# Kernel tuning notes

Measured on AMD Instinct MI355X. Metric: run time of the kernel, lower is better.

The kernel has to match this reference:

```python
import jax, jax.numpy as jnp
import numpy as np
import math

D_MODEL = 1024
NUM_HEADS = 16
D_K = D_MODEL // NUM_HEADS
MAX_SEQ_LEN = 2048
THETA = 10000.0
BATCH = 2
SEQ = 2048


def setup_inputs() -> dict:
    key = jax.random.key(0)
    ks = jax.random.split(key, 5)
    std = math.sqrt(2.0 / (D_MODEL + D_MODEL))
    def w(k):
        return jnp.clip(std * jax.random.normal(k, (D_MODEL, D_MODEL), dtype=jnp.float32), -3 * std, 3 * std)
    return {
        "x": jax.random.normal(ks[0], (BATCH, SEQ, D_MODEL), dtype=jnp.float32),
        "token_positions": jnp.arange(SEQ, dtype=jnp.int32),
        "Wq": w(ks[1]),
        "Wk": w(ks[2]),
        "Wv": w(ks[3]),
        "Wo": w(ks[4]),
    }


def _rope_tables():
    inv_freq = 1.0 / THETA ** (jnp.arange(0, D_K, 2, dtype=jnp.float32) / D_K)  # [d_k/2]
    positions = jnp.arange(MAX_SEQ_LEN, dtype=jnp.float32)[:, None]             # [max_seq, 1]
    angles = positions * inv_freq                                               # [max_seq, d_k/2]
    return jnp.cos(angles), jnp.sin(angles)


def _apply_rope(x, cos, sin):
    # x: [..., seq, d_k]; cos/sin: [seq, d_k/2] (broadcast over leading dims)
    x1, x2 = x[..., ::2], x[..., 1::2]
    r1 = x1 * cos - x2 * sin
    r2 = x1 * sin + x2 * cos
    return jnp.stack((r1, r2), axis=-1).reshape(x.shape)


def reference(x, token_positions, Wq, Wk, Wv, Wo):
    B, S, D = x.shape
    def proj(W):
        y = jnp.einsum('bsd,od->bso', x, W)
        return y.reshape(B, S, NUM_HEADS, D_K).transpose(0, 2, 1, 3)  # [B,H,S,dk]
    q, k, v = proj(Wq), proj(Wk), proj(Wv)

    cos_t, sin_t = _rope_tables()
    cos, sin = cos_t[token_positions], sin_t[token_positions]  # [S, d_k/2]
    q = _apply_rope(q, cos, sin)
    k = _apply_rope(k, cos, sin)

    scores = jnp.einsum('bhqd,bhkd->bhqk', q, k) / math.sqrt(D_K)
    causal = jnp.tril(jnp.ones((S, S), dtype=bool))
    scores = jnp.where(causal, scores, -jnp.inf)
    attn = jax.nn.softmax(scores, axis=-1)
    out = jnp.einsum('bhqk,bhkd->bhqd', attn, v)
    out = out.transpose(0, 2, 1, 3).reshape(B, S, D)
    return jnp.einsum('bsd,od->bso', out, Wo)
```

## Files before the change

### kernel.cpp

```cpp
#include <hip/hip_runtime.h>
#include <hip/hip_bf16.h>


typedef __attribute__((ext_vector_type(8))) short short8;
typedef __attribute__((ext_vector_type(4))) float floatx4;

static __device__ __forceinline__ unsigned short f2bf(float f) {
  __hip_bfloat16 h = __float2bfloat16(f);
  return *(unsigned short*)&h;
}

static __device__ __forceinline__ unsigned int pk2bf(float a, float b) {
  unsigned int ua = __float_as_uint(a) + 0x8000u;
  unsigned int ub = __float_as_uint(b) + 0x8000u;
  return __builtin_amdgcn_perm(ub, ua, 0x07060302u);
}

static __device__ __forceinline__ float fexp2(float x) {
  float r;
  asm("v_exp_f32 %0, %1\n\ts_nop 0" : "=v"(r) : "v"(x));
  return r;
}

static __device__ __forceinline__ void gl2lds16(const unsigned short* g,
                                                unsigned short* l) {
  __builtin_amdgcn_global_load_lds(
      (const __attribute__((address_space(1))) void*)g,
      (__attribute__((address_space(3))) void*)l, 16, 0, 0);
}

__global__ __launch_bounds__(256) void cvt_all(
    const float4* __restrict__ x,  const float4* __restrict__ wq,
    const float4* __restrict__ wk, const float4* __restrict__ wv,
    const float4* __restrict__ wo,
    ushort4* __restrict__ xb,  ushort4* __restrict__ wqb,
    ushort4* __restrict__ wkb, ushort4* __restrict__ wvb,
    ushort4* __restrict__ wob,
    const int* __restrict__ tokpos,
    float* __restrict__ ctab, float* __restrict__ stab) {
  int t = blockIdx.y;
  int i = blockIdx.x * 256 + threadIdx.x;
  if (t == 5) {
    if (i < 65536) {
      int s = i >> 5, f = i & 31;
      float inv = expf(-9.210340371976184f * (float)(2 * f) / 64.0f);
      float ang = (float)tokpos[s] * inv;
      ctab[i] = cosf(ang);
      stab[i] = sinf(ang);
    }
    return;
  }
  const float4* s = (t == 0) ? x : (t == 1) ? wq : (t == 2) ? wk : (t == 3) ? wv : wo;
  ushort4* d = (t == 0) ? xb : (t == 1) ? wqb : (t == 2) ? wkb : (t == 3) ? wvb : wob;
  int n4 = (t == 0) ? 1048576 : 262144;
  if (i < n4) {
    float4 v = s[i];
    ushort4 o;
    o.x = f2bf(v.x); o.y = f2bf(v.y); o.z = f2bf(v.z); o.w = f2bf(v.w);
    d[i] = o;
  }
}

#define GEMM128_BODY(Aptr, Wptr, m0, n0)                                        \
  __shared__ __align__(16) unsigned short lA[128 * 64];                         \
  __shared__ __align__(16) unsigned short lB[128 * 64];                         \
  int tid = threadIdx.x;                                                        \
  int wave = tid >> 6, lane = tid & 63;                                         \
  int wm = wave >> 1, wn = wave & 1;                                            \
  int l15 = lane & 15, quad = lane >> 4;                                        \
  int srow = wave * 32 + (lane >> 3);                   \
  int sch = lane & 7;                                   \
  int fsw = l15 & 7;                                 \
  floatx4 acc[4][4];                                                            \
  _Pragma("unroll") for (int m = 0; m < 4; ++m)                                 \
      _Pragma("unroll") for (int n = 0; n < 4; ++n)                             \
          acc[m][n] = (floatx4){0.f, 0.f, 0.f, 0.f};                            \
  for (int kt = 0; kt < 16; ++kt) {                                             \
    _Pragma("unroll") for (int p = 0; p < 4; ++p) {                             \
      int r = srow + p * 8;                                                     \
      int g = sch ^ (r & 7);                                                    \
      gl2lds16(Aptr + (size_t)(m0 + r) * 1024 + kt * 64 + g * 8,                \
               lA + (wave * 32 + p * 8) * 64);                                  \
      gl2lds16(Wptr + (size_t)(n0 + r) * 1024 + kt * 64 + g * 8,                \
               lB + (wave * 32 + p * 8) * 64);                                  \
    }                                                                           \
    __syncthreads();                                                            \
    _Pragma("unroll") for (int ks = 0; ks < 2; ++ks) {                          \
      short8 af[4], bf[4];                                                      \
      _Pragma("unroll") for (int m = 0; m < 4; ++m)                             \
          af[m] = *(const short8*)(lA + (wm * 64 + m * 16 + l15) * 64 +         \
                                   (((ks * 4 + quad) ^ fsw) * 8));              \
      _Pragma("unroll") for (int n = 0; n < 4; ++n)                             \
          bf[n] = *(const short8*)(lB + (wn * 64 + n * 16 + l15) * 64 +         \
                                   (((ks * 4 + quad) ^ fsw) * 8));              \
      _Pragma("unroll") for (int m = 0; m < 4; ++m)                             \
          _Pragma("unroll") for (int n = 0; n < 4; ++n)                         \
              acc[m][n] = __builtin_amdgcn_mfma_f32_16x16x32_bf16(              \
                  af[m], bf[n], acc[m][n], 0, 0, 0);                            \
    }                                                                           \
    __syncthreads();                                                            \
  }

__global__ __launch_bounds__(256) void qkv_mfma(
    const unsigned short* __restrict__ X,
    const unsigned short* __restrict__ Wq,
    const unsigned short* __restrict__ Wk,
    const unsigned short* __restrict__ Wv,
    const float* __restrict__ ctab, const float* __restrict__ stab,
    unsigned short* __restrict__ Qo, unsigned short* __restrict__ Ko,
    unsigned short* __restrict__ Vo) {
  int mat = blockIdx.z;
  const unsigned short* W = (mat == 0) ? Wq : ((mat == 1) ? Wk : Wv);
  unsigned short* Out = (mat == 0) ? Qo : ((mat == 1) ? Ko : Vo);
  int m0 = blockIdx.x * 128, n0 = blockIdx.y * 128;

  GEMM128_BODY(X, W, m0, n0)

#pragma unroll
  for (int n = 0; n < 4; ++n) {
    int col = n0 + wn * 64 + n * 16 + l15;
    int h = col >> 6;
    int d = col & 63;
    int pi = d >> 1;
    bool odd = (d & 1) != 0;
    size_t hb = (size_t)h * 2048 * 64;
#pragma unroll
    for (int m = 0; m < 4; ++m) {
      int row0 = m0 + wm * 64 + m * 16 + quad * 4;
      int b = row0 >> 11;
      int s0 = row0 & 2047;
      size_t base = (size_t)b * 16 * 2048 * 64 + hb;
      if (mat == 2) {
        ushort4 pv;
        pv.x = f2bf(acc[m][n][0]);
        pv.y = f2bf(acc[m][n][1]);
        pv.z = f2bf(acc[m][n][2]);
        pv.w = f2bf(acc[m][n][3]);
        *(ushort4*)(Out + base + (size_t)d * 2048 + s0) = pv;
      } else {
#pragma unroll
        for (int i = 0; i < 4; ++i) {
          int s = s0 + i;
          float v = acc[m][n][i];
          float p = __shfl_xor(v, 1);
          float c = ctab[s * 32 + pi];
          float sn = stab[s * 32 + pi];
          float res = odd ? fmaf(p, sn, v * c) : fmaf(v, c, -p * sn);
          if (mat == 0) res *= 0.1803368801111204f;
          Out[base + (size_t)s * 64 + d] = f2bf(res);
        }
      }
    }
  }
}

__global__ __launch_bounds__(256) void oproj_mfma(
    const unsigned short* __restrict__ A, const unsigned short* __restrict__ Wo,
    float* __restrict__ Out) {
  __shared__ __align__(16) unsigned short lA[64 * 64];
  __shared__ __align__(16) unsigned short lB[128 * 64];
  int tid = threadIdx.x;
  int wave = tid >> 6, lane = tid & 63;
  int l15 = lane & 15, quad = lane >> 4;
  int rsub = lane >> 3, sch = lane & 7;
  int fsw = l15 & 7;
  int m0 = blockIdx.x * 64, n0 = blockIdx.y * 128;

  floatx4 acc[4][2];
#pragma unroll
  for (int m = 0; m < 4; ++m)
#pragma unroll
    for (int n = 0; n < 2; ++n) acc[m][n] = (floatx4){0.f, 0.f, 0.f, 0.f};

  for (int kt = 0; kt < 16; ++kt) {
#pragma unroll
    for (int p = 0; p < 2; ++p) {
      int r = wave * 16 + p * 8 + rsub;
      int g = sch ^ (r & 7);
      gl2lds16(A + (size_t)(m0 + r) * 1024 + kt * 64 + g * 8,
               lA + (wave * 16 + p * 8) * 64);
    }
#pragma unroll
    for (int p = 0; p < 4; ++p) {
      int r = wave * 32 + p * 8 + rsub;
      int g = sch ^ (r & 7);
      gl2lds16(Wo + (size_t)(n0 + r) * 1024 + kt * 64 + g * 8,
               lB + (wave * 32 + p * 8) * 64);
    }
    __syncthreads();
#pragma unroll
    for (int ks = 0; ks < 2; ++ks) {
      int slot = ((ks * 4 + quad) ^ fsw) * 8;
      short8 af[4], bf[2];
#pragma unroll
      for (int m = 0; m < 4; ++m)
        af[m] = *(const short8*)(lA + (m * 16 + l15) * 64 + slot);
#pragma unroll
      for (int n = 0; n < 2; ++n)
        bf[n] = *(const short8*)(lB + (wave * 32 + n * 16 + l15) * 64 + slot);
#pragma unroll
      for (int m = 0; m < 4; ++m)
#pragma unroll
        for (int n = 0; n < 2; ++n)
          acc[m][n] = __builtin_amdgcn_mfma_f32_16x16x32_bf16(
              af[m], bf[n], acc[m][n], 0, 0, 0);
    }
    __syncthreads();
  }

#pragma unroll
  for (int m = 0; m < 4; ++m) {
#pragma unroll
    for (int n = 0; n < 2; ++n) {
      int col = n0 + wave * 32 + n * 16 + l15;
#pragma unroll
      for (int i = 0; i < 4; ++i) {
        int row = m0 + m * 16 + quad * 4 + i;
        Out[(size_t)row * 1024 + col] = acc[m][n][i];
      }
    }
  }
}

#define LPS 72

__global__ __launch_bounds__(256) void attn_flash(
    const unsigned short* __restrict__ Q, const unsigned short* __restrict__ K,
    const unsigned short* __restrict__ Vt, unsigned short* __restrict__ Oc) {
  __shared__ __align__(16) unsigned short lK[64 * 64];
  __shared__ __align__(16) unsigned short lV[64 * 64];
  __shared__ unsigned short lP[4][16 * LPS];

  int tid = threadIdx.x;
  int wave = tid >> 6, lane = tid & 63;
  int l15 = lane & 15, quad = lane >> 4;

  int xb_ = blockIdx.x;
  int yb_ = blockIdx.y;
  int jb = yb_ >> 3, ib = yb_ & 7;
  int qtile;
  if (jb == 0)      qtile = xb_;
  else if (jb == 1) qtile = 31 - xb_;
  else if (jb == 2) qtile = (15 - xb_) & 31;
  else              qtile = (16 + xb_) & 31;
  int bh = ib * 4 + jb;

  size_t base = (size_t)bh * 2048 * 64;
  int qbase = qtile * 64;

  const unsigned short* qrow = Q + base + (size_t)(qbase + wave * 16 + l15) * 64;
  short8 qb0 = *(const short8*)(qrow + quad * 8);
  short8 qb1 = *(const short8*)(qrow + 32 + quad * 8);

  floatx4 o[4];
  float m_i = -1e30f, l_i = 0.f;
#pragma unroll
  for (int n = 0; n < 4; ++n) o[n] = (floatx4){0.f, 0.f, 0.f, 0.f};

  int r0 = tid >> 3, g = tid & 7;
  int r1 = r0 + 32;
  int e0 = g * 8;
  int sl = (g ^ (r0 & 7)) * 8;
  int fsw = l15 & 7;
  int c0 = (quad ^ fsw) * 8;
  int c1 = ((quad + 4) ^ fsw) * 8;

  const unsigned short* kp = K + base;
  const unsigned short* vp = Vt + base;
  short8 pk0 = *(const short8*)(kp + r0 * 64 + e0);
  short8 pk1 = *(const short8*)(kp + r1 * 64 + e0);
  short8 pv0 = *(const short8*)(vp + (size_t)r0 * 2048 + e0);
  short8 pv1 = *(const short8*)(vp + (size_t)r1 * 2048 + e0);

  for (int kt = 0; kt <= qtile; ++kt) {
    __syncthreads();
    *(short8*)(lK + r0 * 64 + sl) = pk0;
    *(short8*)(lK + r1 * 64 + sl) = pk1;
    *(short8*)(lV + r0 * 64 + sl) = pv0;
    *(short8*)(lV + r1 * 64 + sl) = pv1;
    __syncthreads();

    if (kt < qtile) {
      const unsigned short* kn = K + base + (size_t)(kt + 1) * 4096;
      const unsigned short* vn = Vt + base + (kt + 1) * 64;
      pk0 = *(const short8*)(kn + r0 * 64 + e0);
      pk1 = *(const short8*)(kn + r1 * 64 + e0);
      pv0 = *(const short8*)(vn + (size_t)r0 * 2048 + e0);
      pv1 = *(const short8*)(vn + (size_t)r1 * 2048 + e0);
    }

    float sc[4][4];
#pragma unroll
    for (int sub = 0; sub < 4; ++sub) {
      const unsigned short* kr = lK + (sub * 16 + l15) * 64;
      short8 a0 = *(const short8*)(kr + c0);
      short8 a1 = *(const short8*)(kr + c1);
      floatx4 s = {0.f, 0.f, 0.f, 0.f};
      s = __builtin_amdgcn_mfma_f32_16x16x32_bf16(a0, qb0, s, 0, 0, 0);
      s = __builtin_amdgcn_mfma_f32_16x16x32_bf16(a1, qb1, s, 0, 0, 0);
#pragma unroll
      for (int i = 0; i < 4; ++i) sc[sub][i] = s[i];
    }

    if (kt == qtile) {
      int qin = wave * 16 + l15;
#pragma unroll
      for (int sub = 0; sub < 4; ++sub)
#pragma unroll
        for (int i = 0; i < 4; ++i)
          if (sub * 16 + quad * 4 + i > qin) sc[sub][i] = -1e30f;
    }

    float mb = sc[0][0];
#pragma unroll
    for (int sub = 0; sub < 4; ++sub)
#pragma unroll
      for (int i = 0; i < 4; ++i) mb = fmaxf(mb, sc[sub][i]);
    mb = fmaxf(mb, __shfl_xor(mb, 16));
    mb = fmaxf(mb, __shfl_xor(mb, 32));

    float mn = fmaxf(m_i, mb);
    float al = fexp2(m_i - mn);
    m_i = mn;
    float rs = 0.f;
#pragma unroll
    for (int sub = 0; sub < 4; ++sub)
#pragma unroll
      for (int i = 0; i < 4; ++i) {
        float p = fexp2(sc[sub][i] - mn);
        sc[sub][i] = p;
        rs += p;
      }
    rs += __shfl_xor(rs, 16);
    rs += __shfl_xor(rs, 32);
    l_i = l_i * al + rs;

#pragma unroll
    for (int n = 0; n < 4; ++n) {
      o[n][0] *= al; o[n][1] *= al; o[n][2] *= al; o[n][3] *= al;
    }

    unsigned short* pw = lP[wave] + l15 * LPS;
#pragma unroll
    for (int sub = 0; sub < 4; ++sub) {
      uint2 w;
      w.x = pk2bf(sc[sub][0], sc[sub][1]);
      w.y = pk2bf(sc[sub][2], sc[sub][3]);
      *(uint2*)(pw + sub * 16 + quad * 4) = w;
    }

    const unsigned short* pr = lP[wave] + l15 * LPS + quad * 8;
    short8 pa0 = *(const short8*)(pr);
    short8 pa1 = *(const short8*)(pr + 32);

#pragma unroll
    for (int n = 0; n < 4; ++n) {
      const unsigned short* vr = lV + (n * 16 + l15) * 64;
      short8 vb0 = *(const short8*)(vr + c0);
      short8 vb1 = *(const short8*)(vr + c1);
      o[n] = __builtin_amdgcn_mfma_f32_16x16x32_bf16(vb0, pa0, o[n], 0, 0, 0);
      o[n] = __builtin_amdgcn_mfma_f32_16x16x32_bf16(vb1, pa1, o[n], 0, 0, 0);
    }
  }

  int b = bh >> 4, h = bh & 15;
  float inv = 1.f / l_i;
  int s = qbase + wave * 16 + l15;
  size_t orow = (size_t)(b * 2048 + s) * 1024 + h * 64;
#pragma unroll
  for (int n = 0; n < 4; ++n) {
    uint2 ov;
    ov.x = pk2bf(o[n][0] * inv, o[n][1] * inv);
    ov.y = pk2bf(o[n][2] * inv, o[n][3] * inv);
    *(uint2*)(Oc + orow + n * 16 + quad * 4) = ov;
  }
}

extern "C" void kernel_launch(void* const* d_in, const int* in_sizes, int n_in,
                              void* d_out, int out_size, void* d_ws, size_t ws_size,
                              hipStream_t stream) {
  const float* x  = (const float*)d_in[0];
  const int* tokpos = (const int*)d_in[1];
  const float* Wq = (const float*)d_in[2];
  const float* Wk = (const float*)d_in[3];
  const float* Wv = (const float*)d_in[4];
  const float* Wo = (const float*)d_in[5];
  float* out = (float*)d_out;

  float* ws = (float*)d_ws;
  float* ctab = ws;
  float* stab = ctab + 65536;
  unsigned short* u = (unsigned short*)(stab + 65536);
  unsigned short* Qb  = u;
  unsigned short* Kb  = Qb + 4194304;
  unsigned short* Vb  = Kb + 4194304;
  unsigned short* Oc  = Vb + 4194304;
  unsigned short* xb  = Oc + 4194304;
  unsigned short* Wqb = xb + 4194304;
  unsigned short* Wkb = Wqb + 1048576;
  unsigned short* Wvb = Wkb + 1048576;
  unsigned short* Wob = Wvb + 1048576;

  cvt_all<<<dim3(4096, 6), 256, 0, stream>>>(
      (const float4*)x, (const float4*)Wq, (const float4*)Wk,
      (const float4*)Wv, (const float4*)Wo,
      (ushort4*)xb, (ushort4*)Wqb, (ushort4*)Wkb, (ushort4*)Wvb, (ushort4*)Wob,
      tokpos, ctab, stab);

  qkv_mfma<<<dim3(32, 8, 3), 256, 0, stream>>>(
      xb, Wqb, Wkb, Wvb, ctab, stab, Qb, Kb, Vb);
  attn_flash<<<dim3(32, 32), 256, 0, stream>>>(Qb, Kb, Vb, Oc);
  oproj_mfma<<<dim3(64, 8), 256, 0, stream>>>(Oc, Wob, out);
}
```

Baseline: 190.4 us.

## Load K and V fragments directly from global memory, dropping LDS staging

The attention kernel no longer stages K and V tiles through shared memory with block-wide barriers and register prefetch. Each wave now loads its MFMA operand fragments for K and V^T straight from global memory every iteration. This removes two __syncthreads per tile and the LDS traffic, but each of the four waves now fetches the same K/V data separately, relying on cache for reuse. It also loses the software prefetch of the next tile, so global latency is exposed inside the loop.

```diff
diff --git a/kernel.cpp b/kernel.cpp
--- a/kernel.cpp
+++ b/kernel.cpp
@@ -227,8 +227,6 @@
 __global__ __launch_bounds__(256) void attn_flash(
     const unsigned short* __restrict__ Q, const unsigned short* __restrict__ K,
     const unsigned short* __restrict__ Vt, unsigned short* __restrict__ Oc) {
-  __shared__ __align__(16) unsigned short lK[64 * 64];
-  __shared__ __align__(16) unsigned short lV[64 * 64];
   __shared__ unsigned short lP[4][16 * LPS];
 
   int tid = threadIdx.x;
@@ -257,47 +255,33 @@
 #pragma unroll
   for (int n = 0; n < 4; ++n) o[n] = (floatx4){0.f, 0.f, 0.f, 0.f};
 
-  int r0 = tid >> 3, g = tid & 7;
-  int r1 = r0 + 32;
-  int e0 = g * 8;
-  int sl = (g ^ (r0 & 7)) * 8;
-  int fsw = l15 & 7;
-  int c0 = (quad ^ fsw) * 8;
-  int c1 = ((quad + 4) ^ fsw) * 8;
-
-  const unsigned short* kp = K + base;
-  const unsigned short* vp = Vt + base;
-  short8 pk0 = *(const short8*)(kp + r0 * 64 + e0);
-  short8 pk1 = *(const short8*)(kp + r1 * 64 + e0);
-  short8 pv0 = *(const short8*)(vp + (size_t)r0 * 2048 + e0);
-  short8 pv1 = *(const short8*)(vp + (size_t)r1 * 2048 + e0);
+  const unsigned short* kfrag = K + base + (size_t)(l15)*64 + quad * 8;
+  const unsigned short* vfrag = Vt + base + (size_t)(l15)*2048 + quad * 8;
 
   for (int kt = 0; kt <= qtile; ++kt) {
-    __syncthreads();
-    *(short8*)(lK + r0 * 64 + sl) = pk0;
-    *(short8*)(lK + r1 * 64 + sl) = pk1;
-    *(short8*)(lV + r0 * 64 + sl) = pv0;
-    *(short8*)(lV + r1 * 64 + sl) = pv1;
-    __syncthreads();
-
-    if (kt < qtile) {
-      const unsigned short* kn = K + base + (size_t)(kt + 1) * 4096;
-      const unsigned short* vn = Vt + base + (kt + 1) * 64;
-      pk0 = *(const short8*)(kn + r0 * 64 + e0);
-      pk1 = *(const short8*)(kn + r1 * 64 + e0);
-      pv0 = *(const short8*)(vn + (size_t)r0 * 2048 + e0);
-      pv1 = *(const short8*)(vn + (size_t)r1 * 2048 + e0);
+    int k0 = kt * 64;
+
+    short8 ka0[4], ka1[4];
+#pragma unroll
+    for (int sub = 0; sub < 4; ++sub) {
+      const unsigned short* kr = kfrag + (size_t)(k0 + sub * 16) * 64;
+      ka0[sub] = *(const short8*)(kr);
+      ka1[sub] = *(const short8*)(kr + 32);
+    }
+    short8 va0[4], va1[4];
+#pragma unroll
+    for (int n = 0; n < 4; ++n) {
+      const unsigned short* vr = vfrag + (size_t)(n * 16) * 2048 + k0;
+      va0[n] = *(const short8*)(vr);
+      va1[n] = *(const short8*)(vr + 32);
     }
 
     float sc[4][4];
 #pragma unroll
     for (int sub = 0; sub < 4; ++sub) {
-      const unsigned short* kr = lK + (sub * 16 + l15) * 64;
-      short8 a0 = *(const short8*)(kr + c0);
-      short8 a1 = *(const short8*)(kr + c1);
       floatx4 s = {0.f, 0.f, 0.f, 0.f};
-      s = __builtin_amdgcn_mfma_f32_16x16x32_bf16(a0, qb0, s, 0, 0, 0);
-      s = __builtin_amdgcn_mfma_f32_16x16x32_bf16(a1, qb1, s, 0, 0, 0);
+      s = __builtin_amdgcn_mfma_f32_16x16x32_bf16(ka0[sub], qb0, s, 0, 0, 0);
+      s = __builtin_amdgcn_mfma_f32_16x16x32_bf16(ka1[sub], qb1, s, 0, 0, 0);
 #pragma unroll
       for (int i = 0; i < 4; ++i) sc[sub][i] = s[i];
     }
@@ -355,11 +339,8 @@
 
 #pragma unroll
     for (int n = 0; n < 4; ++n) {
-      const unsigned short* vr = lV + (n * 16 + l15) * 64;
-      short8 vb0 = *(const short8*)(vr + c0);
-      short8 vb1 = *(const short8*)(vr + c1);
-      o[n] = __builtin_amdgcn_mfma_f32_16x16x32_bf16(vb0, pa0, o[n], 0, 0, 0);
-      o[n] = __builtin_amdgcn_mfma_f32_16x16x32_bf16(vb1, pa1, o[n], 0, 0, 0);
+      o[n] = __builtin_amdgcn_mfma_f32_16x16x32_bf16(va0[n], pa0, o[n], 0, 0, 0);
+      o[n] = __builtin_amdgcn_mfma_f32_16x16x32_bf16(va1[n], pa1, o[n], 0, 0, 0);
     }
   }
 
```

Result: slower. 265.2 us (+39.3%).

## Double-buffer K/V tiles in LDS and swizzle P scratch layout

Applied to the files above, without the earlier changes.

The attention loop now keeps two LDS buffers for K and V. The next tile is written into the alternate buffer after the current tile's compute, so each iteration needs one barrier instead of two. The per-wave P scratch also drops its padded stride in favour of an XOR-swizzled 64-wide layout, to cut LDS bank conflicts on the P write and read. The cost is double the K/V LDS footprint, which may lower occupancy.

```diff
diff --git a/kernel.cpp b/kernel.cpp
--- a/kernel.cpp
+++ b/kernel.cpp
@@ -222,14 +222,12 @@
   }
 }
 
-#define LPS 72
-
 __global__ __launch_bounds__(256) void attn_flash(
     const unsigned short* __restrict__ Q, const unsigned short* __restrict__ K,
     const unsigned short* __restrict__ Vt, unsigned short* __restrict__ Oc) {
-  __shared__ __align__(16) unsigned short lK[64 * 64];
-  __shared__ __align__(16) unsigned short lV[64 * 64];
-  __shared__ unsigned short lP[4][16 * LPS];
+  __shared__ __align__(16) unsigned short lK[2][64 * 64];
+  __shared__ __align__(16) unsigned short lV[2][64 * 64];
+  __shared__ __align__(16) unsigned short lP[4][16 * 64];
 
   int tid = threadIdx.x;
   int wave = tid >> 6, lane = tid & 63;
@@ -265,22 +263,27 @@
   int c0 = (quad ^ fsw) * 8;
   int c1 = ((quad + 4) ^ fsw) * 8;
 
-  const unsigned short* kp = K + base;
-  const unsigned short* vp = Vt + base;
-  short8 pk0 = *(const short8*)(kp + r0 * 64 + e0);
-  short8 pk1 = *(const short8*)(kp + r1 * 64 + e0);
-  short8 pv0 = *(const short8*)(vp + (size_t)r0 * 2048 + e0);
-  short8 pv1 = *(const short8*)(vp + (size_t)r1 * 2048 + e0);
+  short8 pk0, pk1, pv0, pv1;
+  {
+    const unsigned short* kp = K + base;
+    const unsigned short* vp = Vt + base;
+    pk0 = *(const short8*)(kp + r0 * 64 + e0);
+    pk1 = *(const short8*)(kp + r1 * 64 + e0);
+    pv0 = *(const short8*)(vp + (size_t)r0 * 2048 + e0);
+    pv1 = *(const short8*)(vp + (size_t)r1 * 2048 + e0);
+    *(short8*)(lK[0] + r0 * 64 + sl) = pk0;
+    *(short8*)(lK[0] + r1 * 64 + sl) = pk1;
+    *(short8*)(lV[0] + r0 * 64 + sl) = pv0;
+    *(short8*)(lV[0] + r1 * 64 + sl) = pv1;
+  }
+  __syncthreads();
 
   for (int kt = 0; kt <= qtile; ++kt) {
-    __syncthreads();
-    *(short8*)(lK + r0 * 64 + sl) = pk0;
-    *(short8*)(lK + r1 * 64 + sl) = pk1;
-    *(short8*)(lV + r0 * 64 + sl) = pv0;
-    *(short8*)(lV + r1 * 64 + sl) = pv1;
-    __syncthreads();
-
-    if (kt < qtile) {
+    const unsigned short* kcur = lK[kt & 1];
+    const unsigned short* vcur = lV[kt & 1];
+    bool more = (kt < qtile);
+
+    if (more) {
       const unsigned short* kn = K + base + (size_t)(kt + 1) * 4096;
       const unsigned short* vn = Vt + base + (kt + 1) * 64;
       pk0 = *(const short8*)(kn + r0 * 64 + e0);
@@ -292,7 +295,7 @@
     float sc[4][4];
 #pragma unroll
     for (int sub = 0; sub < 4; ++sub) {
-      const unsigned short* kr = lK + (sub * 16 + l15) * 64;
+      const unsigned short* kr = kcur + (sub * 16 + l15) * 64;
       short8 a0 = *(const short8*)(kr + c0);
       short8 a1 = *(const short8*)(kr + c1);
       floatx4 s = {0.f, 0.f, 0.f, 0.f};
@@ -340,26 +343,37 @@
       o[n][0] *= al; o[n][1] *= al; o[n][2] *= al; o[n][3] *= al;
     }
 
-    unsigned short* pw = lP[wave] + l15 * LPS;
+    unsigned short* pw = lP[wave] + l15 * 64;
 #pragma unroll
     for (int sub = 0; sub < 4; ++sub) {
+      int pc = (((sub << 1) | (quad >> 1)) ^ fsw) * 8 + (quad & 1) * 4;
       uint2 w;
       w.x = pk2bf(sc[sub][0], sc[sub][1]);
       w.y = pk2bf(sc[sub][2], sc[sub][3]);
-      *(uint2*)(pw + sub * 16 + quad * 4) = w;
-    }
-
-    const unsigned short* pr = lP[wave] + l15 * LPS + quad * 8;
-    short8 pa0 = *(const short8*)(pr);
-    short8 pa1 = *(const short8*)(pr + 32);
+      *(uint2*)(pw + pc) = w;
+    }
+
+    const unsigned short* pr = lP[wave] + l15 * 64;
+    short8 pa0 = *(const short8*)(pr + c0);
+    short8 pa1 = *(const short8*)(pr + c1);
 
 #pragma unroll
     for (int n = 0; n < 4; ++n) {
-      const unsigned short* vr = lV + (n * 16 + l15) * 64;
+      const unsigned short* vr = vcur + (n * 16 + l15) * 64;
       short8 vb0 = *(const short8*)(vr + c0);
       short8 vb1 = *(const short8*)(vr + c1);
       o[n] = __builtin_amdgcn_mfma_f32_16x16x32_bf16(vb0, pa0, o[n], 0, 0, 0);
       o[n] = __builtin_amdgcn_mfma_f32_16x16x32_bf16(vb1, pa1, o[n], 0, 0, 0);
+    }
+
+    if (more) {
+      unsigned short* kd = lK[(kt + 1) & 1];
+      unsigned short* vd = lV[(kt + 1) & 1];
+      *(short8*)(kd + r0 * 64 + sl) = pk0;
+      *(short8*)(kd + r1 * 64 + sl) = pk1;
+      *(short8*)(vd + r0 * 64 + sl) = pv0;
+      *(short8*)(vd + r1 * 64 + sl) = pv1;
+      __syncthreads();
     }
   }
 
```

Result: slower. 205.3 us (+7.8%).
